# Optimization experiments

Hardware: AMD Instinct MI355X
Metric: run time of the kernel (lower is better)

## Reference

```python
import jax, jax.numpy as jnp
import numpy as np

N_NODES = 100000
N_EDGES = 1600000
D_IN = 128
D_OUT = 128
NEG_SLOPE = 0.01  # torch F.leaky_relu default


def setup_inputs() -> dict:
    key = jax.random.key(0)
    k1, k2, k3, k4, k5 = jax.random.split(key, 5)
    h = jax.random.normal(k1, (N_NODES, D_IN), dtype=jnp.float32)
    # nn.Linear default init scale ~ 1/sqrt(fan_in)
    W = jax.random.normal(k2, (D_IN, D_OUT), dtype=jnp.float32) / np.sqrt(D_IN)
    attn_w = jax.random.normal(k3, (2 * D_OUT,), dtype=jnp.float32) / np.sqrt(2 * D_OUT)
    edge_src = jax.random.randint(k4, (N_EDGES,), 0, N_NODES, dtype=jnp.int32)
    edge_dst = jax.random.randint(k5, (N_EDGES,), 0, N_NODES, dtype=jnp.int32)
    return {"h": h, "W": W, "attn_w": attn_w, "edge_src": edge_src, "edge_dst": edge_dst}


def reference(h, W, attn_w, edge_src, edge_dst):
    n = h.shape[0]
    d = W.shape[1]
    z = h @ W                                   # [N, d]
    # attention_func(cat([z_src, z_dst])) == z_src @ a[:d] + z_dst @ a[d:]
    s_src = z @ attn_w[:d]                      # [N]
    s_dst = z @ attn_w[d:]                      # [N]
    e = jax.nn.leaky_relu(s_src[edge_src] + s_dst[edge_dst], NEG_SLOPE)  # [E]
    # segment softmax over incoming edges of each dst node
    m = jax.ops.segment_max(e, edge_dst, num_segments=n)   # [N], -inf for empty
    ex = jnp.exp(e - m[edge_dst])                           # [E]
    denom = jax.ops.segment_sum(ex, edge_dst, num_segments=n)  # [N]
    alpha = ex / denom[edge_dst]                             # [E]
    # weighted neighbor sum: sum_j alpha_ij * z_j
    out = jax.ops.segment_sum(alpha[:, None] * z[edge_src], edge_dst, num_segments=n)
    return out
```

## Files before the change

### kernel.cpp

```cpp
#include <hip/hip_runtime.h>

#define D 128
#define NEG_SLOPE 0.01f
#define BSHIFT 7
#define B1 1024
#define SCHUNK 4096
#define SLOT 2560

typedef __attribute__((ext_vector_type(8))) short short8;
typedef __attribute__((ext_vector_type(4))) float floatx4;

__device__ __forceinline__ unsigned f2bf_rne(float x) {
    unsigned u = __float_as_uint(x);
    return (u + 0x7fffu + ((u >> 16) & 1u)) >> 16;
}
#define BF_LO(u) __uint_as_float((u) << 16)
#define BF_HI(u) __uint_as_float((u) & 0xffff0000u)

__global__ __launch_bounds__(1024) void sort_prep(
        const int* __restrict__ esrc, const int* __restrict__ edst,
        int* __restrict__ gcur, int* __restrict__ pairs, int E, int NSORT,
        const float* __restrict__ W, unsigned short* __restrict__ whi,
        unsigned short* __restrict__ wlo) {
    __shared__ int cnt[B1], exc[B1], gbs[B1], cur[B1];
    __shared__ int spk[SCHUNK];
    __shared__ unsigned short sbkt[SCHUNK];
    __shared__ int wtot[16];
    const int t = threadIdx.x;

    if ((int)blockIdx.x >= NSORT) {
        const int idx = (blockIdx.x - NSORT) * 1024 + t;
        const int j    = idx & 7;
        const int lane = (idx >> 3) & 63;
        const int tk   = idx >> 9;
        const int kk = tk & 3, ct = tk >> 2;
        const int k = kk * 32 + (lane >> 4) * 8 + j;
        const int n = ct * 16 + (lane & 15);
        const float x = W[k * D + n];
        const unsigned hi = f2bf_rne(x);
        const float hf = __uint_as_float(hi << 16);
        whi[idx] = (unsigned short)hi;
        wlo[idx] = (unsigned short)(__float_as_uint(x - hf) >> 16);
        return;
    }

    const int lane = t & 63, wv = t >> 6;
    cnt[t] = 0; cur[t] = 0;
    __syncthreads();

    const int e0 = blockIdx.x * SCHUNK;
    const int n  = min(SCHUNK, E - e0);

    int pk[4], bk[4];
    const int i0 = t * 4;
    if (i0 + 3 < n) {
        const int4 dv = *(const int4*)&edst[e0 + i0];
        const int4 sv = *(const int4*)&esrc[e0 + i0];
        const int dd[4] = {dv.x, dv.y, dv.z, dv.w};
        const int ss[4] = {sv.x, sv.y, sv.z, sv.w};
#pragma unroll
        for (int k = 0; k < 4; ++k) {
            bk[k] = dd[k] >> BSHIFT;
            pk[k] = (ss[k] << BSHIFT) | (dd[k] & 127);
            atomicAdd(&cnt[bk[k]], 1);
        }
    } else {
#pragma unroll
        for (int k = 0; k < 4; ++k) {
            const int i = i0 + k;
            if (i < n) {
                const int d = edst[e0 + i];
                const int s = esrc[e0 + i];
                bk[k] = d >> BSHIFT;
                pk[k] = (s << BSHIFT) | (d & 127);
                atomicAdd(&cnt[bk[k]], 1);
            } else {
                bk[k] = -1;
            }
        }
    }
    __syncthreads();

    const int c = cnt[t];
    int incl = c;
#pragma unroll
    for (int o = 1; o < 64; o <<= 1) {
        int v = __shfl_up(incl, o, 64);
        if (lane >= o) incl += v;
    }
    if (lane == 63) wtot[wv] = incl;
    __syncthreads();
    int wpre = 0;
#pragma unroll
    for (int i = 0; i < 16; ++i) wpre += (i < wv) ? wtot[i] : 0;
    exc[t] = wpre + incl - c;
    if (c > 0) gbs[t] = atomicAdd(&gcur[t], c);
    __syncthreads();

#pragma unroll
    for (int k = 0; k < 4; ++k) {
        if (bk[k] >= 0) {
            const int p = exc[bk[k]] + atomicAdd(&cur[bk[k]], 1);
            spk[p]  = pk[k];
            sbkt[p] = (unsigned short)bk[k];
        }
    }
    __syncthreads();

    for (int i = t; i < n; i += 1024) {
        const int b = sbkt[i];
        const int off = gbs[b] + (i - exc[b]);
        if (off < SLOT) pairs[b * SLOT + off] = spk[i];
    }
}

__global__ __launch_bounds__(256, 3) void fine_gemm(
        const int* __restrict__ pairs, const int* __restrict__ gcur,
        int* __restrict__ beg, int* __restrict__ ncnt, int* __restrict__ adj,
        int NFINE,
        const float* __restrict__ h, const unsigned short* __restrict__ whi,
        const unsigned short* __restrict__ wlo, const float* __restrict__ aw,
        unsigned short* __restrict__ z, float* __restrict__ s_src,
        float* __restrict__ s_dst, int N) {
    __shared__ int cnt[4][128], woff[4][128], cur[4][128];
    __shared__ int sc[128];
    const int t = threadIdx.x;
    const int lane = t & 63;

    if ((int)blockIdx.x < NFINE) {
        const int b = blockIdx.x;
        const int base = b << BSHIFT;
        const int nd = min(128, N - base);
        const int wv = t >> 6;
        const int s0 = b * SLOT;
        const int e1 = s0 + min(gcur[b], SLOT);
        for (int i = t; i < 512; i += 256) { (&cnt[0][0])[i] = 0; (&cur[0][0])[i] = 0; }
        __syncthreads();
        for (int i = s0 + t; i < e1; i += 256)
            atomicAdd(&cnt[wv][pairs[i] & 127], 1);
        __syncthreads();
        if (t < 128) {
            const int c0 = cnt[0][t], c1 = cnt[1][t], c2 = cnt[2][t];
            woff[0][t] = 0; woff[1][t] = c0; woff[2][t] = c0 + c1; woff[3][t] = c0 + c1 + c2;
            sc[t] = c0 + c1 + c2 + cnt[3][t];
        }
        __syncthreads();
        for (int off = 1; off < 128; off <<= 1) {
            int v = (t < 128 && t >= off) ? sc[t - off] : 0;
            __syncthreads();
            if (t < 128) sc[t] += v;
            __syncthreads();
        }
        if (t < 128) {
            const int tot = cnt[0][t] + cnt[1][t] + cnt[2][t] + cnt[3][t];
            const int excl = sc[t] - tot;
            if (t < nd) { beg[base + t] = s0 + excl; ncnt[base + t] = tot; }
            woff[0][t] += excl; woff[1][t] += excl; woff[2][t] += excl; woff[3][t] += excl;
        }
        __syncthreads();
        for (int i = s0 + t; i < e1; i += 256) {
            const int pkv = pairs[i];
            const int d = pkv & 127;
            const int pos = s0 + woff[wv][d] + atomicAdd(&cur[wv][d], 1);
            adj[pos] = pkv >> BSHIFT;
        }
        return;
    }

    const int gbid = blockIdx.x - NFINE;
    const int quad = lane >> 4, l16 = lane & 15;
    const int rowbase = gbid * 64 + (t >> 6) * 16;
    const int arow = min(rowbase + l16, N - 1);
    const float* __restrict__ hrow = h + (size_t)arow * D;

    float4 hx[8];
#pragma unroll
    for (int kk = 0; kk < 4; ++kk) {
        const int k0 = kk * 32 + quad * 8;
        hx[kk * 2]     = *(const float4*)&hrow[k0];
        hx[kk * 2 + 1] = *(const float4*)&hrow[k0 + 4];
    }
    union { short8 v; unsigned short u[8]; } ahi[4], alo[4];
#pragma unroll
    for (int kk = 0; kk < 4; ++kk) {
        const float xs[8] = {hx[kk*2].x, hx[kk*2].y, hx[kk*2].z, hx[kk*2].w,
                             hx[kk*2+1].x, hx[kk*2+1].y, hx[kk*2+1].z, hx[kk*2+1].w};
#pragma unroll
        for (int i = 0; i < 8; ++i) {
            const unsigned hi = f2bf_rne(xs[i]);
            const float hf = __uint_as_float(hi << 16);
            ahi[kk].u[i] = (unsigned short)hi;
            alo[kk].u[i] = (unsigned short)(__float_as_uint(xs[i] - hf) >> 16);
        }
    }

    floatx4 acc[8];
#pragma unroll
    for (int ct = 0; ct < 8; ++ct) acc[ct] = (floatx4){0.f, 0.f, 0.f, 0.f};

#pragma unroll
    for (int kk = 0; kk < 4; ++kk)
#pragma unroll
        for (int ct = 0; ct < 8; ++ct) {
            const int fo = ((ct * 4 + kk) * 64 + lane) * 8;
            short8 bhi = *(const short8*)&whi[fo];
            short8 blo = *(const short8*)&wlo[fo];
            acc[ct] = __builtin_amdgcn_mfma_f32_16x16x32_bf16(ahi[kk].v, bhi, acc[ct], 0, 0, 0);
            acc[ct] = __builtin_amdgcn_mfma_f32_16x16x32_bf16(alo[kk].v, bhi, acc[ct], 0, 0, 0);
            acc[ct] = __builtin_amdgcn_mfma_f32_16x16x32_bf16(ahi[kk].v, blo, acc[ct], 0, 0, 0);
        }

#pragma unroll
    for (int ct = 0; ct < 8; ++ct)
#pragma unroll
        for (int reg = 0; reg < 4; ++reg) {
            int r = rowbase + quad * 4 + reg;
            if (r < N)
                z[(size_t)r * D + ct * 16 + l16] = (unsigned short)f2bf_rne(acc[ct][reg]);
        }

    float ps[4] = {0.f, 0.f, 0.f, 0.f}, pd[4] = {0.f, 0.f, 0.f, 0.f};
#pragma unroll
    for (int ct = 0; ct < 8; ++ct) {
        float as = aw[ct * 16 + l16];
        float ad = aw[128 + ct * 16 + l16];
#pragma unroll
        for (int reg = 0; reg < 4; ++reg) {
            ps[reg] = fmaf(acc[ct][reg], as, ps[reg]);
            pd[reg] = fmaf(acc[ct][reg], ad, pd[reg]);
        }
    }
#pragma unroll
    for (int reg = 0; reg < 4; ++reg)
#pragma unroll
        for (int o = 1; o < 16; o <<= 1) {
            ps[reg] += __shfl_xor(ps[reg], o, 64);
            pd[reg] += __shfl_xor(pd[reg], o, 64);
        }
    if (l16 == 0) {
#pragma unroll
        for (int reg = 0; reg < 4; ++reg) {
            int r = rowbase + quad * 4 + reg;
            if (r < N) { s_src[r] = ps[reg]; s_dst[r] = pd[reg]; }
        }
    }
}

__global__ __launch_bounds__(256) void aggregate(const unsigned short* __restrict__ z,
                                                 const float* __restrict__ s_src,
                                                 const float* __restrict__ s_dst,
                                                 const int* __restrict__ beg_,
                                                 const int* __restrict__ ncnt_,
                                                 const int* __restrict__ adj,
                                                 float* __restrict__ out, int N) {
    const int lane = threadIdx.x & 63;
    const int half = lane >> 5;
    const int l32  = lane & 31;
    const int q2   = l32 >> 4;
    const int l16  = lane & 15;
    const int hb   = half << 5;
    const int pairBase = blockIdx.x * 8 + (threadIdx.x >> 6) * 2;
    if (pairBase >= N) return;
    const int nodeA = pairBase, nodeB = pairBase + 1;
    const int cA = ncnt_[nodeA], bA = beg_[nodeA];
    int cB = 0, bB = 0;
    if (nodeB < N) { cB = ncnt_[nodeB]; bB = beg_[nodeB]; }

    auto fma8 = [&](float* ac, float w, const uint4& v) {
        ac[0] = fmaf(w, BF_LO(v.x), ac[0]); ac[1] = fmaf(w, BF_HI(v.x), ac[1]);
        ac[2] = fmaf(w, BF_LO(v.y), ac[2]); ac[3] = fmaf(w, BF_HI(v.y), ac[3]);
        ac[4] = fmaf(w, BF_LO(v.z), ac[4]); ac[5] = fmaf(w, BF_HI(v.z), ac[5]);
        ac[6] = fmaf(w, BF_LO(v.w), ac[6]); ac[7] = fmaf(w, BF_HI(v.w), ac[7]);
    };

    if (max(cA, cB) <= 32) {
        const int myn = pairBase + half;
        const int mb  = half ? bB : bA;
        const int mc  = half ? cB : cA;
        const float sd = s_dst[myn < N ? myn : 0];
        int s = 0; float e = -INFINITY;
        if (l32 < mc) {
            s = adj[mb + l32];
            float tt = s_src[s] + sd;
            e = (tt >= 0.f) ? tt : NEG_SLOPE * tt;
        }
        uint4 g0, g1, g2, g3;
        {
            const int s0_ = __shfl(s, hb + 0 + q2, 64);
            const int s1_ = __shfl(s, hb + 2 + q2, 64);
            const int s2_ = __shfl(s, hb + 4 + q2, 64);
            const int s3_ = __shfl(s, hb + 6 + q2, 64);
            g0 = *(const uint4*)&z[(size_t)s0_ * D + l16 * 8];
            g1 = *(const uint4*)&z[(size_t)s1_ * D + l16 * 8];
            g2 = *(const uint4*)&z[(size_t)s2_ * D + l16 * 8];
            g3 = *(const uint4*)&z[(size_t)s3_ * D + l16 * 8];
        }

        float mx = e;
#pragma unroll
        for (int o = 16; o; o >>= 1) mx = fmaxf(mx, __shfl_xor(mx, o, 64));
        float ex = (l32 < mc) ? __expf(e - mx) : 0.f;
        float sum = ex;
#pragma unroll
        for (int o = 16; o; o >>= 1) sum += __shfl_xor(sum, o, 64);
        const float inv = (mc > 0) ? 1.f / sum : 0.f;
        const float w = ex * inv;

        float a[8] = {0.f,0.f,0.f,0.f,0.f,0.f,0.f,0.f};
        float bacc[8] = {0.f,0.f,0.f,0.f,0.f,0.f,0.f,0.f};
        int jj = 0;
        while (true) {
            const int nj = jj + 8;
            const bool more = nj < mc;
            uint4 n0, n1, n2, n3;
            if (more) {
                const int t0 = __shfl(s, hb + nj + 0 + q2, 64);
                const int t1 = __shfl(s, hb + nj + 2 + q2, 64);
                const int t2 = __shfl(s, hb + nj + 4 + q2, 64);
                const int t3 = __shfl(s, hb + nj + 6 + q2, 64);
                n0 = *(const uint4*)&z[(size_t)t0 * D + l16 * 8];
                n1 = *(const uint4*)&z[(size_t)t1 * D + l16 * 8];
                n2 = *(const uint4*)&z[(size_t)t2 * D + l16 * 8];
                n3 = *(const uint4*)&z[(size_t)t3 * D + l16 * 8];
            }
            {
                float w0 = __shfl(w, hb + jj + 0 + q2, 64);
                float w1 = __shfl(w, hb + jj + 2 + q2, 64);
                float w2 = __shfl(w, hb + jj + 4 + q2, 64);
                float w3 = __shfl(w, hb + jj + 6 + q2, 64);
                w0 = (jj + 0 + q2 < mc) ? w0 : 0.f;
                w1 = (jj + 2 + q2 < mc) ? w1 : 0.f;
                w2 = (jj + 4 + q2 < mc) ? w2 : 0.f;
                w3 = (jj + 6 + q2 < mc) ? w3 : 0.f;
                fma8(a, w0, g0); fma8(bacc, w1, g1);
                fma8(a, w2, g2); fma8(bacc, w3, g3);
            }
            if (!more) break;
            g0 = n0; g1 = n1; g2 = n2; g3 = n3;
            jj = nj;
        }
#pragma unroll
        for (int i = 0; i < 8; ++i) {
            a[i] += bacc[i];
            a[i] += __shfl_xor(a[i], 16, 64);
        }
        if (q2 == 0 && myn < N) {
            float* o = &out[(size_t)myn * D + l16 * 8];
            *(float4*)o       = make_float4(a[0], a[1], a[2], a[3]);
            *(float4*)(o + 4) = make_float4(a[4], a[5], a[6], a[7]);
        }
        return;
    }

    const int q = lane >> 4;
    for (int which = 0; which < 2; ++which) {
        const int myn = which ? nodeB : nodeA;
        if (myn >= N) break;
        const int mb = which ? bB : bA;
        const int mc = which ? cB : cA;
        const float sd = s_dst[myn];
        float a[8] = {0.f,0.f,0.f,0.f,0.f,0.f,0.f,0.f};
        float bacc[8] = {0.f,0.f,0.f,0.f,0.f,0.f,0.f,0.f};
        float mx = -INFINITY;
        for (int j = lane; j < mc; j += 64) {
            float tt = s_src[adj[mb + j]] + sd;
            tt = (tt >= 0.f) ? tt : NEG_SLOPE * tt;
            mx = fmaxf(mx, tt);
        }
#pragma unroll
        for (int o = 32; o; o >>= 1) mx = fmaxf(mx, __shfl_xor(mx, o, 64));
        float sum = 0.f;
        for (int j = lane; j < mc; j += 64) {
            float tt = s_src[adj[mb + j]] + sd;
            tt = (tt >= 0.f) ? tt : NEG_SLOPE * tt;
            sum += __expf(tt - mx);
        }
#pragma unroll
        for (int o = 32; o; o >>= 1) sum += __shfl_xor(sum, o, 64);
        const float inv = (mc > 0) ? 1.f / sum : 0.f;
        for (int base2 = 0; base2 < mc; base2 += 64) {
            const int cc = min(64, mc - base2);
            int s = 0; float w = 0.f;
            if (lane < cc) {
                s = adj[mb + base2 + lane];
                float tt = s_src[s] + sd;
                tt = (tt >= 0.f) ? tt : NEG_SLOPE * tt;
                w = __expf(tt - mx) * inv;
            }
            for (int jj = 0; jj < cc; jj += 8) {
                const int ja = jj + q;
                const int jb = ja + 4;
                float wa = __shfl(w, ja, 64); int sa = __shfl(s, ja, 64);
                float wb = __shfl(w, jb, 64); int sb = __shfl(s, jb, 64);
                wa = (ja < cc) ? wa : 0.f;
                wb = (jb < cc) ? wb : 0.f;
                uint4 za = *(const uint4*)&z[(size_t)sa * D + l16 * 8];
                uint4 zb = *(const uint4*)&z[(size_t)sb * D + l16 * 8];
                fma8(a, wa, za);
                fma8(bacc, wb, zb);
            }
        }
#pragma unroll
        for (int i = 0; i < 8; ++i) {
            a[i] += bacc[i];
            a[i] += __shfl_xor(a[i], 16, 64);
            a[i] += __shfl_xor(a[i], 32, 64);
        }
        if (q == 0) {
            float* o = &out[(size_t)myn * D + l16 * 8];
            *(float4*)o       = make_float4(a[0], a[1], a[2], a[3]);
            *(float4*)(o + 4) = make_float4(a[4], a[5], a[6], a[7]);
        }
    }
}

extern "C" void kernel_launch(void* const* d_in, const int* in_sizes, int n_in,
                              void* d_out, int out_size, void* d_ws, size_t ws_size,
                              hipStream_t stream) {
    const float* h    = (const float*)d_in[0];
    const float* W    = (const float*)d_in[1];
    const float* aw   = (const float*)d_in[2];
    const int*   esrc = (const int*)d_in[3];
    const int*   edst = (const int*)d_in[4];
    float* out = (float*)d_out;

    const int N = in_sizes[0] / D;
    const int E = in_sizes[3];
    const int NB1   = (N + 127) >> BSHIFT;
    const int NSORT = (E + SCHUNK - 1) / SCHUNK;
    const int NGEMM = (N + 63) / 64;

    char* p = (char*)d_ws;
    auto carve = [&](size_t bytes) {
        void* r = (void*)p;
        p += (bytes + 255) & ~size_t(255);
        return r;
    };
    unsigned short* z = (unsigned short*)carve(size_t(N) * D * sizeof(unsigned short));
    float* s_src  = (float*)carve(size_t(N) * sizeof(float));
    float* s_dst  = (float*)carve(size_t(N) * sizeof(float));
    int*   pairs  = (int*)carve(size_t(NB1) * SLOT * sizeof(int));
    int*   adj    = (int*)carve(size_t(NB1) * SLOT * sizeof(int));
    int*   beg    = (int*)carve(size_t(N) * sizeof(int));
    int*   ncnt   = (int*)carve(size_t(N) * sizeof(int));
    int*   gcur   = (int*)carve(size_t(B1) * sizeof(int));
    unsigned short* whi = (unsigned short*)carve(16384 * sizeof(unsigned short));
    unsigned short* wlo = (unsigned short*)carve(16384 * sizeof(unsigned short));
    (void)ws_size; (void)n_in; (void)out_size;

    hipMemsetAsync(gcur, 0, B1 * sizeof(int), stream);
    sort_prep<<<NSORT + 16, 1024, 0, stream>>>(esrc, edst, gcur, pairs, E, NSORT,
                                               W, whi, wlo);
    fine_gemm<<<NB1 + NGEMM, 256, 0, stream>>>(pairs, gcur, beg, ncnt, adj, NB1,
                                               h, whi, wlo, aw, z, s_src, s_dst, N);
    aggregate<<<(N + 7) / 8, 256, 0, stream>>>(z, s_src, s_dst, beg, ncnt, adj, out, N);
}
```

Before: 215.4 us.

## Fuse fine bucket sort into aggregation kernel using shared-memory adjacency

```diff
diff --git a/kernel.cpp b/kernel.cpp
--- a/kernel.cpp
+++ b/kernel.cpp
@@ -114,62 +114,16 @@
     }
 }
 
-__global__ __launch_bounds__(256, 3) void fine_gemm(
-        const int* __restrict__ pairs, const int* __restrict__ gcur,
-        int* __restrict__ beg, int* __restrict__ ncnt, int* __restrict__ adj,
-        int NFINE,
-        const float* __restrict__ h, const unsigned short* __restrict__ whi,
-        const unsigned short* __restrict__ wlo, const float* __restrict__ aw,
-        unsigned short* __restrict__ z, float* __restrict__ s_src,
-        float* __restrict__ s_dst, int N) {
-    __shared__ int cnt[4][128], woff[4][128], cur[4][128];
-    __shared__ int sc[128];
+__global__ __launch_bounds__(256, 3) void gemm_zs(const float* __restrict__ h,
+                                                  const unsigned short* __restrict__ whi,
+                                                  const unsigned short* __restrict__ wlo,
+                                                  const float* __restrict__ aw,
+                                                  unsigned short* __restrict__ z,
+                                                  float* __restrict__ s_src,
+                                                  float* __restrict__ s_dst, int N) {
     const int t = threadIdx.x;
-    const int lane = t & 63;
-
-    if ((int)blockIdx.x < NFINE) {
-        const int b = blockIdx.x;
-        const int base = b << BSHIFT;
-        const int nd = min(128, N - base);
-        const int wv = t >> 6;
-        const int s0 = b * SLOT;
-        const int e1 = s0 + min(gcur[b], SLOT);
-        for (int i = t; i < 512; i += 256) { (&cnt[0][0])[i] = 0; (&cur[0][0])[i] = 0; }
-        __syncthreads();
-        for (int i = s0 + t; i < e1; i += 256)
-            atomicAdd(&cnt[wv][pairs[i] & 127], 1);
-        __syncthreads();
-        if (t < 128) {
-            const int c0 = cnt[0][t], c1 = cnt[1][t], c2 = cnt[2][t];
-            woff[0][t] = 0; woff[1][t] = c0; woff[2][t] = c0 + c1; woff[3][t] = c0 + c1 + c2;
-            sc[t] = c0 + c1 + c2 + cnt[3][t];
-        }
-        __syncthreads();
-        for (int off = 1; off < 128; off <<= 1) {
-            int v = (t < 128 && t >= off) ? sc[t - off] : 0;
-            __syncthreads();
-            if (t < 128) sc[t] += v;
-            __syncthreads();
-        }
-        if (t < 128) {
-            const int tot = cnt[0][t] + cnt[1][t] + cnt[2][t] + cnt[3][t];
-            const int excl = sc[t] - tot;
-            if (t < nd) { beg[base + t] = s0 + excl; ncnt[base + t] = tot; }
-            woff[0][t] += excl; woff[1][t] += excl; woff[2][t] += excl; woff[3][t] += excl;
-        }
-        __syncthreads();
-        for (int i = s0 + t; i < e1; i += 256) {
-            const int pkv = pairs[i];
-            const int d = pkv & 127;
-            const int pos = s0 + woff[wv][d] + atomicAdd(&cur[wv][d], 1);
-            adj[pos] = pkv >> BSHIFT;
-        }
-        return;
-    }
-
-    const int gbid = blockIdx.x - NFINE;
-    const int quad = lane >> 4, l16 = lane & 15;
-    const int rowbase = gbid * 64 + (t >> 6) * 16;
+    const int lane = t & 63, quad = lane >> 4, l16 = lane & 15;
+    const int rowbase = blockIdx.x * 64 + (t >> 6) * 16;
     const int arow = min(rowbase + l16, N - 1);
     const float* __restrict__ hrow = h + (size_t)arow * D;
 
@@ -246,25 +200,68 @@
     }
 }
 
-__global__ __launch_bounds__(256) void aggregate(const unsigned short* __restrict__ z,
+__global__ __launch_bounds__(512) void agg_fused(const unsigned short* __restrict__ z,
                                                  const float* __restrict__ s_src,
                                                  const float* __restrict__ s_dst,
-                                                 const int* __restrict__ beg_,
-                                                 const int* __restrict__ ncnt_,
-                                                 const int* __restrict__ adj,
+                                                 const int* __restrict__ pairs,
+                                                 const int* __restrict__ gcur,
                                                  float* __restrict__ out, int N) {
-    const int lane = threadIdx.x & 63;
+    __shared__ int cnt[8][128], woff[8][128], cur[8][128];
+    __shared__ int sc[128], tot[128];
+    __shared__ int lsrc[SLOT];
+    const int b = blockIdx.x;
+    const int base = b << BSHIFT;
+    const int nd = min(128, N - base);
+    const int t = threadIdx.x;
+    const int wv = t >> 6;
+    const int lane = t & 63;
+    const int s0 = b * SLOT;
+    const int nb = min(gcur[b], SLOT);
+
+    for (int i = t; i < 1024; i += 512) { (&cnt[0][0])[i] = 0; (&cur[0][0])[i] = 0; }
+    __syncthreads();
+    int pk[5];
+#pragma unroll
+    for (int k = 0; k < 5; ++k) {
+        const int i = t + k * 512;
+        pk[k] = (i < nb) ? pairs[s0 + i] : -1;
+        if (pk[k] >= 0) atomicAdd(&cnt[wv][pk[k] & 127], 1);
+    }
+    __syncthreads();
+    if (t < 128) {
+        int run = 0;
+#pragma unroll
+        for (int i = 0; i < 8; ++i) { woff[i][t] = run; run += cnt[i][t]; }
+        tot[t] = run; sc[t] = run;
+    }
+    __syncthreads();
+    for (int off = 1; off < 128; off <<= 1) {
+        int v = (t < 128 && t >= off) ? sc[t - off] : 0;
+        __syncthreads();
+        if (t < 128) sc[t] += v;
+        __syncthreads();
+    }
+    if (t < 128) {
+        const int excl = sc[t] - tot[t];
+#pragma unroll
+        for (int i = 0; i < 8; ++i) woff[i][t] += excl;
+    }
+    __syncthreads();
+#pragma unroll
+    for (int k = 0; k < 5; ++k) {
+        if (pk[k] >= 0) {
+            const int d = pk[k] & 127;
+            const int pos = woff[wv][d] + atomicAdd(&cur[wv][d], 1);
+            lsrc[pos] = pk[k] >> BSHIFT;
+        }
+    }
+    __syncthreads();
+
     const int half = lane >> 5;
     const int l32  = lane & 31;
     const int q2   = l32 >> 4;
     const int l16  = lane & 15;
     const int hb   = half << 5;
-    const int pairBase = blockIdx.x * 8 + (threadIdx.x >> 6) * 2;
-    if (pairBase >= N) return;
-    const int nodeA = pairBase, nodeB = pairBase + 1;
-    const int cA = ncnt_[nodeA], bA = beg_[nodeA];
-    int cB = 0, bB = 0;
-    if (nodeB < N) { cB = ncnt_[nodeB]; bB = beg_[nodeB]; }
 
     auto fma8 = [&](float* ac, float w, const uint4& v) {
         ac[0] = fmaf(w, BF_LO(v.x), ac[0]); ac[1] = fmaf(w, BF_HI(v.x), ac[1]);
@@ -273,143 +270,153 @@
         ac[6] = fmaf(w, BF_LO(v.w), ac[6]); ac[7] = fmaf(w, BF_HI(v.w), ac[7]);
     };
 
-    if (max(cA, cB) <= 32) {
-        const int myn = pairBase + half;
-        const int mb  = half ? bB : bA;
-        const int mc  = half ? cB : cA;
-        const float sd = s_dst[myn < N ? myn : 0];
-        int s = 0; float e = -INFINITY;
-        if (l32 < mc) {
-            s = adj[mb + l32];
-            float tt = s_src[s] + sd;
-            e = (tt >= 0.f) ? tt : NEG_SLOPE * tt;
-        }
-        uint4 g0, g1, g2, g3;
-        {
-            const int s0_ = __shfl(s, hb + 0 + q2, 64);
-            const int s1_ = __shfl(s, hb + 2 + q2, 64);
-            const int s2_ = __shfl(s, hb + 4 + q2, 64);
-            const int s3_ = __shfl(s, hb + 6 + q2, 64);
-            g0 = *(const uint4*)&z[(size_t)s0_ * D + l16 * 8];
-            g1 = *(const uint4*)&z[(size_t)s1_ * D + l16 * 8];
-            g2 = *(const uint4*)&z[(size_t)s2_ * D + l16 * 8];
-            g3 = *(const uint4*)&z[(size_t)s3_ * D + l16 * 8];
-        }
-
-        float mx = e;
-#pragma unroll
-        for (int o = 16; o; o >>= 1) mx = fmaxf(mx, __shfl_xor(mx, o, 64));
-        float ex = (l32 < mc) ? __expf(e - mx) : 0.f;
-        float sum = ex;
-#pragma unroll
-        for (int o = 16; o; o >>= 1) sum += __shfl_xor(sum, o, 64);
-        const float inv = (mc > 0) ? 1.f / sum : 0.f;
-        const float w = ex * inv;
-
-        float a[8] = {0.f,0.f,0.f,0.f,0.f,0.f,0.f,0.f};
-        float bacc[8] = {0.f,0.f,0.f,0.f,0.f,0.f,0.f,0.f};
-        int jj = 0;
-        while (true) {
-            const int nj = jj + 8;
-            const bool more = nj < mc;
-            uint4 n0, n1, n2, n3;
-            if (more) {
-                const int t0 = __shfl(s, hb + nj + 0 + q2, 64);
-                const int t1 = __shfl(s, hb + nj + 2 + q2, 64);
-                const int t2 = __shfl(s, hb + nj + 4 + q2, 64);
-                const int t3 = __shfl(s, hb + nj + 6 + q2, 64);
-                n0 = *(const uint4*)&z[(size_t)t0 * D + l16 * 8];
-                n1 = *(const uint4*)&z[(size_t)t1 * D + l16 * 8];
-                n2 = *(const uint4*)&z[(size_t)t2 * D + l16 * 8];
-                n3 = *(const uint4*)&z[(size_t)t3 * D + l16 * 8];
-            }
+    for (int dd = wv * 2; dd < nd; dd += 16) {
+        const int dA = dd, dB = dd + 1;
+        const int cA = tot[dA];
+        const int bgA = sc[dA] - cA;
+        int cB = 0, bgB = 0;
+        if (dB < nd) { cB = tot[dB]; bgB = sc[dB] - cB; }
+
+        if (max(cA, cB) <= 32) {
+            const int myd = dd + half;
+            const int valid = myd < nd;
+            const int mb  = half ? bgB : bgA;
+            const int mc  = half ? cB : cA;
+            const int myn = base + (valid ? myd : 0);
+            const float sd = s_dst[myn];
+            int s = 0; float e = -INFINITY;
+            if (l32 < mc) {
+                s = lsrc[mb + l32];
+                float tt = s_src[s] + sd;
+                e = (tt >= 0.f) ? tt : NEG_SLOPE * tt;
+            }
+            uint4 g0, g1, g2, g3;
             {
-                float w0 = __shfl(w, hb + jj + 0 + q2, 64);
-                float w1 = __shfl(w, hb + jj + 2 + q2, 64);
-                float w2 = __shfl(w, hb + jj + 4 + q2, 64);
-                float w3 = __shfl(w, hb + jj + 6 + q2, 64);
-                w0 = (jj + 0 + q2 < mc) ? w0 : 0.f;
-                w1 = (jj + 2 + q2 < mc) ? w1 : 0.f;
-                w2 = (jj + 4 + q2 < mc) ? w2 : 0.f;
-                w3 = (jj + 6 + q2 < mc) ? w3 : 0.f;
-                fma8(a, w0, g0); fma8(bacc, w1, g1);
-                fma8(a, w2, g2); fma8(bacc, w3, g3);
-            }
-            if (!more) break;
-            g0 = n0; g1 = n1; g2 = n2; g3 = n3;
-            jj = nj;
-        }
-#pragma unroll
-        for (int i = 0; i < 8; ++i) {
-            a[i] += bacc[i];
-            a[i] += __shfl_xor(a[i], 16, 64);
-        }
-        if (q2 == 0 && myn < N) {
-            float* o = &out[(size_t)myn * D + l16 * 8];
-            *(float4*)o       = make_float4(a[0], a[1], a[2], a[3]);
-            *(float4*)(o + 4) = make_float4(a[4], a[5], a[6], a[7]);
-        }
-        return;
-    }
-
-    const int q = lane >> 4;
-    for (int which = 0; which < 2; ++which) {
-        const int myn = which ? nodeB : nodeA;
-        if (myn >= N) break;
-        const int mb = which ? bB : bA;
-        const int mc = which ? cB : cA;
-        const float sd = s_dst[myn];
-        float a[8] = {0.f,0.f,0.f,0.f,0.f,0.f,0.f,0.f};
-        float bacc[8] = {0.f,0.f,0.f,0.f,0.f,0.f,0.f,0.f};
-        float mx = -INFINITY;
-        for (int j = lane; j < mc; j += 64) {
-            float tt = s_src[adj[mb + j]] + sd;
-            tt = (tt >= 0.f) ? tt : NEG_SLOPE * tt;
-            mx = fmaxf(mx, tt);
-        }
-#pragma unroll
-        for (int o = 32; o; o >>= 1) mx = fmaxf(mx, __shfl_xor(mx, o, 64));
-        float sum = 0.f;
-        for (int j = lane; j < mc; j += 64) {
-            float tt = s_src[adj[mb + j]] + sd;
-            tt = (tt >= 0.f) ? tt : NEG_SLOPE * tt;
-            sum += __expf(tt - mx);
-        }
-#pragma unroll
-        for (int o = 32; o; o >>= 1) sum += __shfl_xor(sum, o, 64);
-        const float inv = (mc > 0) ? 1.f / sum : 0.f;
-        for (int base2 = 0; base2 < mc; base2 += 64) {
-            const int cc = min(64, mc - base2);
-            int s = 0; float w = 0.f;
-            if (lane < cc) {
-                s = adj[mb + base2 + lane];
-                float tt = s_src[s] + sd;
+                const int s0_ = __shfl(s, hb + 0 + q2, 64);
+                const int s1_ = __shfl(s, hb + 2 + q2, 64);
+                const int s2_ = __shfl(s, hb + 4 + q2, 64);
+                const int s3_ = __shfl(s, hb + 6 + q2, 64);
+                g0 = *(const uint4*)&z[(size_t)s0_ * D + l16 * 8];
+                g1 = *(const uint4*)&z[(size_t)s1_ * D + l16 * 8];
+                g2 = *(const uint4*)&z[(size_t)s2_ * D + l16 * 8];
+                g3 = *(const uint4*)&z[(size_t)s3_ * D + l16 * 8];
+            }
+            float mx = e;
+#pragma unroll
+            for (int o = 16; o; o >>= 1) mx = fmaxf(mx, __shfl_xor(mx, o, 64));
+            float ex = (l32 < mc) ? __expf(e - mx) : 0.f;
+            float sum = ex;
+#pragma unroll
+            for (int o = 16; o; o >>= 1) sum += __shfl_xor(sum, o, 64);
+            const float inv = (mc > 0) ? 1.f / sum : 0.f;
+            const float w = ex * inv;
+
+            float a[8] = {0.f,0.f,0.f,0.f,0.f,0.f,0.f,0.f};
+            float bacc[8] = {0.f,0.f,0.f,0.f,0.f,0.f,0.f,0.f};
+            int jj = 0;
+            while (true) {
+                const int nj = jj + 8;
+                const bool more = nj < mc;
+                uint4 n0, n1, n2, n3;
+                if (more) {
+                    const int t0 = __shfl(s, hb + nj + 0 + q2, 64);
+                    const int t1 = __shfl(s, hb + nj + 2 + q2, 64);
+                    const int t2 = __shfl(s, hb + nj + 4 + q2, 64);
+                    const int t3 = __shfl(s, hb + nj + 6 + q2, 64);
+                    n0 = *(const uint4*)&z[(size_t)t0 * D + l16 * 8];
+                    n1 = *(const uint4*)&z[(size_t)t1 * D + l16 * 8];
+                    n2 = *(const uint4*)&z[(size_t)t2 * D + l16 * 8];
+                    n3 = *(const uint4*)&z[(size_t)t3 * D + l16 * 8];
+                }
+                {
+                    float w0 = __shfl(w, hb + jj + 0 + q2, 64);
+                    float w1 = __shfl(w, hb + jj + 2 + q2, 64);
+                    float w2 = __shfl(w, hb + jj + 4 + q2, 64);
+                    float w3 = __shfl(w, hb + jj + 6 + q2, 64);
+                    w0 = (jj + 0 + q2 < mc) ? w0 : 0.f;
+                    w1 = (jj + 2 + q2 < mc) ? w1 : 0.f;
+                    w2 = (jj + 4 + q2 < mc) ? w2 : 0.f;
+                    w3 = (jj + 6 + q2 < mc) ? w3 : 0.f;
+                    fma8(a, w0, g0); fma8(bacc, w1, g1);
+                    fma8(a, w2, g2); fma8(bacc, w3, g3);
+                }
+                if (!more) break;
+                g0 = n0; g1 = n1; g2 = n2; g3 = n3;
+                jj = nj;
+            }
+#pragma unroll
+            for (int i = 0; i < 8; ++i) {
+                a[i] += bacc[i];
+                a[i] += __shfl_xor(a[i], 16, 64);
+            }
+            if (q2 == 0 && valid) {
+                float* o = &out[(size_t)(base + myd) * D + l16 * 8];
+                *(float4*)o       = make_float4(a[0], a[1], a[2], a[3]);
+                *(float4*)(o + 4) = make_float4(a[4], a[5], a[6], a[7]);
+            }
+            continue;
+        }
+
+        const int q = lane >> 4;
+        for (int which = 0; which < 2; ++which) {
+            const int myd = which ? dB : dA;
+            if (myd >= nd) break;
+            const int mb = which ? bgB : bgA;
+            const int mc = which ? cB : cA;
+            const int myn = base + myd;
+            const float sd = s_dst[myn];
+            float a[8] = {0.f,0.f,0.f,0.f,0.f,0.f,0.f,0.f};
+            float bacc[8] = {0.f,0.f,0.f,0.f,0.f,0.f,0.f,0.f};
+            float mx = -INFINITY;
+            for (int j = lane; j < mc; j += 64) {
+                float tt = s_src[lsrc[mb + j]] + sd;
                 tt = (tt >= 0.f) ? tt : NEG_SLOPE * tt;
-                w = __expf(tt - mx) * inv;
-            }
-            for (int jj = 0; jj < cc; jj += 8) {
-                const int ja = jj + q;
-                const int jb = ja + 4;
-                float wa = __shfl(w, ja, 64); int sa = __shfl(s, ja, 64);
-                float wb = __shfl(w, jb, 64); int sb = __shfl(s, jb, 64);
-                wa = (ja < cc) ? wa : 0.f;
-                wb = (jb < cc) ? wb : 0.f;
-                uint4 za = *(const uint4*)&z[(size_t)sa * D + l16 * 8];
-                uint4 zb = *(const uint4*)&z[(size_t)sb * D + l16 * 8];
-                fma8(a, wa, za);
-                fma8(bacc, wb, zb);
-            }
-        }
-#pragma unroll
-        for (int i = 0; i < 8; ++i) {
-            a[i] += bacc[i];
-            a[i] += __shfl_xor(a[i], 16, 64);
-            a[i] += __shfl_xor(a[i], 32, 64);
-        }
-        if (q == 0) {
-            float* o = &out[(size_t)myn * D + l16 * 8];
-            *(float4*)o       = make_float4(a[0], a[1], a[2], a[3]);
-            *(float4*)(o + 4) = make_float4(a[4], a[5], a[6], a[7]);
+                mx = fmaxf(mx, tt);
+            }
+#pragma unroll
+            for (int o = 32; o; o >>= 1) mx = fmaxf(mx, __shfl_xor(mx, o, 64));
+            float sum = 0.f;
+            for (int j = lane; j < mc; j += 64) {
+                float tt = s_src[lsrc[mb + j]] + sd;
+                tt = (tt >= 0.f) ? tt : NEG_SLOPE * tt;
+                sum += __expf(tt - mx);
+            }
+#pragma unroll
+            for (int o = 32; o; o >>= 1) sum += __shfl_xor(sum, o, 64);
+            const float inv = (mc > 0) ? 1.f / sum : 0.f;
+            for (int base2 = 0; base2 < mc; base2 += 64) {
+                const int cc = min(64, mc - base2);
+                int s = 0; float w = 0.f;
+                if (lane < cc) {
+                    s = lsrc[mb + base2 + lane];
+                    float tt = s_src[s] + sd;
+                    tt = (tt >= 0.f) ? tt : NEG_SLOPE * tt;
+                    w = __expf(tt - mx) * inv;
+                }
+                for (int jj = 0; jj < cc; jj += 8) {
+                    const int ja = jj + q;
+                    const int jb = ja + 4;
+                    float wa = __shfl(w, ja, 64); int sa = __shfl(s, ja, 64);
+                    float wb = __shfl(w, jb, 64); int sb = __shfl(s, jb, 64);
+                    wa = (ja < cc) ? wa : 0.f;
+                    wb = (jb < cc) ? wb : 0.f;
+                    uint4 za = *(const uint4*)&z[(size_t)sa * D + l16 * 8];
+                    uint4 zb = *(const uint4*)&z[(size_t)sb * D + l16 * 8];
+                    fma8(a, wa, za);
+                    fma8(bacc, wb, zb);
+                }
+            }
+#pragma unroll
+            for (int i = 0; i < 8; ++i) {
+                a[i] += bacc[i];
+                a[i] += __shfl_xor(a[i], 16, 64);
+                a[i] += __shfl_xor(a[i], 32, 64);
+            }
+            if (q == 0) {
+                float* o = &out[(size_t)myn * D + l16 * 8];
+                *(float4*)o       = make_float4(a[0], a[1], a[2], a[3]);
+                *(float4*)(o + 4) = make_float4(a[4], a[5], a[6], a[7]);
+            }
         }
     }
 }
@@ -440,9 +447,6 @@
     float* s_src  = (float*)carve(size_t(N) * sizeof(float));
     float* s_dst  = (float*)carve(size_t(N) * sizeof(float));
     int*   pairs  = (int*)carve(size_t(NB1) * SLOT * sizeof(int));
-    int*   adj    = (int*)carve(size_t(NB1) * SLOT * sizeof(int));
-    int*   beg    = (int*)carve(size_t(N) * sizeof(int));
-    int*   ncnt   = (int*)carve(size_t(N) * sizeof(int));
     int*   gcur   = (int*)carve(size_t(B1) * sizeof(int));
     unsigned short* whi = (unsigned short*)carve(16384 * sizeof(unsigned short));
     unsigned short* wlo = (unsigned short*)carve(16384 * sizeof(unsigned short));
@@ -451,7 +455,6 @@
     hipMemsetAsync(gcur, 0, B1 * sizeof(int), stream);
     sort_prep<<<NSORT + 16, 1024, 0, stream>>>(esrc, edst, gcur, pairs, E, NSORT,
                                                W, whi, wlo);
-    fine_gemm<<<NB1 + NGEMM, 256, 0, stream>>>(pairs, gcur, beg, ncnt, adj, NB1,
-                                               h, whi, wlo, aw, z, s_src, s_dst, N);
-    aggregate<<<(N + 7) / 8, 256, 0, stream>>>(z, s_src, s_dst, beg, ncnt, adj, out, N);
+    gemm_zs<<<NGEMM, 256, 0, stream>>>(h, whi, wlo, aw, z, s_src, s_dst, N);
+    agg_fused<<<NB1, 512, 0, stream>>>(z, s_src, s_dst, pairs, gcur, out, N);
 }
```

Result: slower. 223.7 us (+3.9%).

## Split aggregation by column slice across XCDs for L2-local z gathers

Applied to the files above, without the earlier changes.

```diff
diff --git a/kernel.cpp b/kernel.cpp
--- a/kernel.cpp
+++ b/kernel.cpp
@@ -6,6 +6,7 @@
 #define B1 1024
 #define SCHUNK 4096
 #define SLOT 2560
+#define NXCD 8
 
 typedef __attribute__((ext_vector_type(8))) short short8;
 typedef __attribute__((ext_vector_type(4))) float floatx4;
@@ -246,25 +247,26 @@
     }
 }
 
-__global__ __launch_bounds__(256) void aggregate(const unsigned short* __restrict__ z,
-                                                 const float* __restrict__ s_src,
-                                                 const float* __restrict__ s_dst,
-                                                 const int* __restrict__ beg_,
-                                                 const int* __restrict__ ncnt_,
-                                                 const int* __restrict__ adj,
-                                                 float* __restrict__ out, int N) {
-    const int lane = threadIdx.x & 63;
+__global__ __launch_bounds__(256) void aggregate_cs(const unsigned short* __restrict__ z,
+                                                    const float* __restrict__ s_src,
+                                                    const float* __restrict__ s_dst,
+                                                    const int* __restrict__ beg_,
+                                                    const int* __restrict__ ncnt_,
+                                                    const int* __restrict__ adj,
+                                                    float* __restrict__ out, int N) {
+    const int cs   = blockIdx.x & (NXCD - 1);
+    const int b    = blockIdx.x >> 3;
+    const int base = b << BSHIFT;
+    const int nd   = min(128, N - base);
+    const int t    = threadIdx.x;
+    const int lane = t & 63;
+    const int wv   = t >> 6;
     const int half = lane >> 5;
     const int l32  = lane & 31;
-    const int q2   = l32 >> 4;
-    const int l16  = lane & 15;
     const int hb   = half << 5;
-    const int pairBase = blockIdx.x * 8 + (threadIdx.x >> 6) * 2;
-    if (pairBase >= N) return;
-    const int nodeA = pairBase, nodeB = pairBase + 1;
-    const int cA = ncnt_[nodeA], bA = beg_[nodeA];
-    int cB = 0, bB = 0;
-    if (nodeB < N) { cB = ncnt_[nodeB]; bB = beg_[nodeB]; }
+    const int eidx = l32 >> 1;
+    const int ecol = l32 & 1;
+    const int coff = cs * 16 + ecol * 8;
 
     auto fma8 = [&](float* ac, float w, const uint4& v) {
         ac[0] = fmaf(w, BF_LO(v.x), ac[0]); ac[1] = fmaf(w, BF_HI(v.x), ac[1]);
@@ -273,143 +275,114 @@
         ac[6] = fmaf(w, BF_LO(v.w), ac[6]); ac[7] = fmaf(w, BF_HI(v.w), ac[7]);
     };
 
-    if (max(cA, cB) <= 32) {
-        const int myn = pairBase + half;
-        const int mb  = half ? bB : bA;
-        const int mc  = half ? cB : cA;
-        const float sd = s_dst[myn < N ? myn : 0];
-        int s = 0; float e = -INFINITY;
-        if (l32 < mc) {
-            s = adj[mb + l32];
-            float tt = s_src[s] + sd;
-            e = (tt >= 0.f) ? tt : NEG_SLOPE * tt;
-        }
-        uint4 g0, g1, g2, g3;
-        {
-            const int s0_ = __shfl(s, hb + 0 + q2, 64);
-            const int s1_ = __shfl(s, hb + 2 + q2, 64);
-            const int s2_ = __shfl(s, hb + 4 + q2, 64);
-            const int s3_ = __shfl(s, hb + 6 + q2, 64);
-            g0 = *(const uint4*)&z[(size_t)s0_ * D + l16 * 8];
-            g1 = *(const uint4*)&z[(size_t)s1_ * D + l16 * 8];
-            g2 = *(const uint4*)&z[(size_t)s2_ * D + l16 * 8];
-            g3 = *(const uint4*)&z[(size_t)s3_ * D + l16 * 8];
-        }
-
-        float mx = e;
-#pragma unroll
-        for (int o = 16; o; o >>= 1) mx = fmaxf(mx, __shfl_xor(mx, o, 64));
-        float ex = (l32 < mc) ? __expf(e - mx) : 0.f;
-        float sum = ex;
-#pragma unroll
-        for (int o = 16; o; o >>= 1) sum += __shfl_xor(sum, o, 64);
-        const float inv = (mc > 0) ? 1.f / sum : 0.f;
-        const float w = ex * inv;
-
-        float a[8] = {0.f,0.f,0.f,0.f,0.f,0.f,0.f,0.f};
-        float bacc[8] = {0.f,0.f,0.f,0.f,0.f,0.f,0.f,0.f};
-        int jj = 0;
-        while (true) {
-            const int nj = jj + 8;
-            const bool more = nj < mc;
-            uint4 n0, n1, n2, n3;
-            if (more) {
-                const int t0 = __shfl(s, hb + nj + 0 + q2, 64);
-                const int t1 = __shfl(s, hb + nj + 2 + q2, 64);
-                const int t2 = __shfl(s, hb + nj + 4 + q2, 64);
-                const int t3 = __shfl(s, hb + nj + 6 + q2, 64);
-                n0 = *(const uint4*)&z[(size_t)t0 * D + l16 * 8];
-                n1 = *(const uint4*)&z[(size_t)t1 * D + l16 * 8];
-                n2 = *(const uint4*)&z[(size_t)t2 * D + l16 * 8];
-                n3 = *(const uint4*)&z[(size_t)t3 * D + l16 * 8];
-            }
-            {
-                float w0 = __shfl(w, hb + jj + 0 + q2, 64);
-                float w1 = __shfl(w, hb + jj + 2 + q2, 64);
-                float w2 = __shfl(w, hb + jj + 4 + q2, 64);
-                float w3 = __shfl(w, hb + jj + 6 + q2, 64);
-                w0 = (jj + 0 + q2 < mc) ? w0 : 0.f;
-                w1 = (jj + 2 + q2 < mc) ? w1 : 0.f;
-                w2 = (jj + 4 + q2 < mc) ? w2 : 0.f;
-                w3 = (jj + 6 + q2 < mc) ? w3 : 0.f;
-                fma8(a, w0, g0); fma8(bacc, w1, g1);
-                fma8(a, w2, g2); fma8(bacc, w3, g3);
-            }
-            if (!more) break;
-            g0 = n0; g1 = n1; g2 = n2; g3 = n3;
-            jj = nj;
-        }
-#pragma unroll
-        for (int i = 0; i < 8; ++i) {
-            a[i] += bacc[i];
-            a[i] += __shfl_xor(a[i], 16, 64);
-        }
-        if (q2 == 0 && myn < N) {
-            float* o = &out[(size_t)myn * D + l16 * 8];
-            *(float4*)o       = make_float4(a[0], a[1], a[2], a[3]);
-            *(float4*)(o + 4) = make_float4(a[4], a[5], a[6], a[7]);
-        }
-        return;
-    }
-
-    const int q = lane >> 4;
-    for (int which = 0; which < 2; ++which) {
-        const int myn = which ? nodeB : nodeA;
-        if (myn >= N) break;
-        const int mb = which ? bB : bA;
-        const int mc = which ? cB : cA;
-        const float sd = s_dst[myn];
-        float a[8] = {0.f,0.f,0.f,0.f,0.f,0.f,0.f,0.f};
-        float bacc[8] = {0.f,0.f,0.f,0.f,0.f,0.f,0.f,0.f};
-        float mx = -INFINITY;
-        for (int j = lane; j < mc; j += 64) {
-            float tt = s_src[adj[mb + j]] + sd;
-            tt = (tt >= 0.f) ? tt : NEG_SLOPE * tt;
-            mx = fmaxf(mx, tt);
-        }
-#pragma unroll
-        for (int o = 32; o; o >>= 1) mx = fmaxf(mx, __shfl_xor(mx, o, 64));
-        float sum = 0.f;
-        for (int j = lane; j < mc; j += 64) {
-            float tt = s_src[adj[mb + j]] + sd;
-            tt = (tt >= 0.f) ? tt : NEG_SLOPE * tt;
-            sum += __expf(tt - mx);
-        }
-#pragma unroll
-        for (int o = 32; o; o >>= 1) sum += __shfl_xor(sum, o, 64);
-        const float inv = (mc > 0) ? 1.f / sum : 0.f;
-        for (int base2 = 0; base2 < mc; base2 += 64) {
-            const int cc = min(64, mc - base2);
-            int s = 0; float w = 0.f;
-            if (lane < cc) {
-                s = adj[mb + base2 + lane];
+    for (int dd = wv * 2; dd < nd; dd += 8) {
+        const int dA = dd, dB = dd + 1;
+        const int cA = ncnt_[base + dA];
+        const int bA = beg_[base + dA];
+        int cB = 0, bB = 0;
+        if (dB < nd) { cB = ncnt_[base + dB]; bB = beg_[base + dB]; }
+
+        if (max(cA, cB) <= 32) {
+            const int myd = dd + half;
+            const int valid = myd < nd;
+            const int mb = half ? bB : bA;
+            const int mc = half ? cB : cA;
+            const int myn = base + (valid ? myd : 0);
+            const float sd = s_dst[myn];
+            int s = 0; float e = -INFINITY;
+            if (l32 < mc) {
+                s = adj[mb + l32];
                 float tt = s_src[s] + sd;
+                e = (tt >= 0.f) ? tt : NEG_SLOPE * tt;
+            }
+            float mx = e;
+#pragma unroll
+            for (int o = 16; o; o >>= 1) mx = fmaxf(mx, __shfl_xor(mx, o, 64));
+            float ex = (l32 < mc) ? __expf(e - mx) : 0.f;
+            float sum = ex;
+#pragma unroll
+            for (int o = 16; o; o >>= 1) sum += __shfl_xor(sum, o, 64);
+            const float inv = (mc > 0) ? 1.f / sum : 0.f;
+            const float w = ex * inv;
+
+            float a8[8] = {0.f,0.f,0.f,0.f,0.f,0.f,0.f,0.f};
+#pragma unroll
+            for (int jj = 0; jj < 32; jj += 16) {
+                if (jj >= mc) break;
+                const int e2 = jj + eidx;
+                float we = __shfl(w, hb + e2, 64);
+                int   se = __shfl(s, hb + e2, 64);
+                we = (e2 < mc) ? we : 0.f;
+                const uint4 v = *(const uint4*)&z[(size_t)se * D + coff];
+                fma8(a8, we, v);
+            }
+#pragma unroll
+            for (int o = 2; o <= 16; o <<= 1)
+#pragma unroll
+                for (int i = 0; i < 8; ++i) a8[i] += __shfl_xor(a8[i], o, 64);
+            if (eidx == 0 && valid) {
+                float* o = &out[(size_t)myn * D + coff];
+                *(float4*)o       = make_float4(a8[0], a8[1], a8[2], a8[3]);
+                *(float4*)(o + 4) = make_float4(a8[4], a8[5], a8[6], a8[7]);
+            }
+            continue;
+        }
+
+        const int feidx = lane >> 1;
+        const int fcoff = cs * 16 + (lane & 1) * 8;
+        for (int which = 0; which < 2; ++which) {
+            const int myd = which ? dB : dA;
+            if (myd >= nd) break;
+            const int mb = which ? bB : bA;
+            const int mc = which ? cB : cA;
+            const int myn = base + myd;
+            const float sd = s_dst[myn];
+            float mx = -INFINITY;
+            for (int j = lane; j < mc; j += 64) {
+                float tt = s_src[adj[mb + j]] + sd;
                 tt = (tt >= 0.f) ? tt : NEG_SLOPE * tt;
-                w = __expf(tt - mx) * inv;
-            }
-            for (int jj = 0; jj < cc; jj += 8) {
-                const int ja = jj + q;
-                const int jb = ja + 4;
-                float wa = __shfl(w, ja, 64); int sa = __shfl(s, ja, 64);
-                float wb = __shfl(w, jb, 64); int sb = __shfl(s, jb, 64);
-                wa = (ja < cc) ? wa : 0.f;
-                wb = (jb < cc) ? wb : 0.f;
-                uint4 za = *(const uint4*)&z[(size_t)sa * D + l16 * 8];
-                uint4 zb = *(const uint4*)&z[(size_t)sb * D + l16 * 8];
-                fma8(a, wa, za);
-                fma8(bacc, wb, zb);
-            }
-        }
-#pragma unroll
-        for (int i = 0; i < 8; ++i) {
-            a[i] += bacc[i];
-            a[i] += __shfl_xor(a[i], 16, 64);
-            a[i] += __shfl_xor(a[i], 32, 64);
-        }
-        if (q == 0) {
-            float* o = &out[(size_t)myn * D + l16 * 8];
-            *(float4*)o       = make_float4(a[0], a[1], a[2], a[3]);
-            *(float4*)(o + 4) = make_float4(a[4], a[5], a[6], a[7]);
+                mx = fmaxf(mx, tt);
+            }
+#pragma unroll
+            for (int o = 32; o; o >>= 1) mx = fmaxf(mx, __shfl_xor(mx, o, 64));
+            float sum = 0.f;
+            for (int j = lane; j < mc; j += 64) {
+                float tt = s_src[adj[mb + j]] + sd;
+                tt = (tt >= 0.f) ? tt : NEG_SLOPE * tt;
+                sum += __expf(tt - mx);
+            }
+#pragma unroll
+            for (int o = 32; o; o >>= 1) sum += __shfl_xor(sum, o, 64);
+            const float inv = (mc > 0) ? 1.f / sum : 0.f;
+
+            float a8[8] = {0.f,0.f,0.f,0.f,0.f,0.f,0.f,0.f};
+            for (int b2 = 0; b2 < mc; b2 += 64) {
+                const int cc = min(64, mc - b2);
+                int s = 0; float w = 0.f;
+                if (lane < cc) {
+                    s = adj[mb + b2 + lane];
+                    float tt = s_src[s] + sd;
+                    tt = (tt >= 0.f) ? tt : NEG_SLOPE * tt;
+                    w = __expf(tt - mx) * inv;
+                }
+                for (int jj = 0; jj < cc; jj += 32) {
+                    const int e2 = jj + feidx;
+                    float we = __shfl(w, e2 & 63, 64);
+                    int   se = __shfl(s, e2 & 63, 64);
+                    we = (e2 < cc) ? we : 0.f;
+                    const uint4 v = *(const uint4*)&z[(size_t)se * D + fcoff];
+                    fma8(a8, we, v);
+                }
+            }
+#pragma unroll
+            for (int o = 2; o <= 32; o <<= 1)
+#pragma unroll
+                for (int i = 0; i < 8; ++i) a8[i] += __shfl_xor(a8[i], o, 64);
+            if (feidx == 0) {
+                float* o = &out[(size_t)myn * D + fcoff];
+                *(float4*)o       = make_float4(a8[0], a8[1], a8[2], a8[3]);
+                *(float4*)(o + 4) = make_float4(a8[4], a8[5], a8[6], a8[7]);
+            }
         }
     }
 }
@@ -453,5 +426,5 @@
                                                W, whi, wlo);
     fine_gemm<<<NB1 + NGEMM, 256, 0, stream>>>(pairs, gcur, beg, ncnt, adj, NB1,
                                                h, whi, wlo, aw, z, s_src, s_dst, N);
-    aggregate<<<(N + 7) / 8, 256, 0, stream>>>(z, s_src, s_dst, beg, ncnt, adj, out, N);
+    aggregate_cs<<<NB1 * NXCD, 256, 0, stream>>>(z, s_src, s_dst, beg, ncnt, adj, out, N);
 }
```

Result: slower. 394.4 us (+83.1%).
